# Optimization experiments

Measured on AMD Instinct MI355X. Metric: run time of the kernel, lower is better.

The kernel has to match this reference:

```python
import jax, jax.numpy as jnp
import numpy as np

N, H, W, PD, HID, NH = 2, 64, 64, 16, 128, 4
EPS = 1e-5


def _bn(x, g, b):
    # training-mode BatchNorm over (N, H, W) with biased variance, channels last
    m = jnp.mean(x, axis=(0, 1, 2), keepdims=True)
    v = jnp.var(x, axis=(0, 1, 2), keepdims=True)
    return (x - m) * jax.lax.rsqrt(v + EPS) * g + b


def _mha(x, in_w, in_b, out_w, out_b, nh):
    # torch nn.MultiheadAttention (batch_first) with packed qkv in_proj
    B, S, E = x.shape
    hd = E // nh
    q, k, v = jnp.split(x @ in_w.T + in_b, 3, axis=-1)
    def heads(t):
        return t.reshape(B, S, nh, hd).transpose(0, 2, 1, 3)  # B,nh,S,hd
    q, k, v = heads(q), heads(k), heads(v)
    a = jax.nn.softmax(jnp.einsum('bnqd,bnkd->bnqk', q, k) / np.float32(np.sqrt(hd)), axis=-1)
    o = jnp.einsum('bnqk,bnkd->bnqd', a, v).transpose(0, 2, 1, 3).reshape(B, S, E)
    return o @ out_w.T + out_b


def setup_inputs():
    key = jax.random.key(0)
    ks = jax.random.split(key, 32)
    def r(i, shape, s=0.1):
        return jax.random.normal(ks[i], shape, dtype=jnp.float32) * s
    mask = (jnp.arange(W) % 2) == 0  # alternating columns kept, M = W//2
    return {
        'kspace': jax.random.normal(ks[0], (N, 2, H, W), dtype=jnp.float32),
        'mask': mask,
        'pre_conv_w': r(1, (PD, 2), 0.5), 'pre_conv_b': r(2, (PD,)),
        'pre_pe_H': r(3, (H, PD)), 'pre_pe_W': r(4, (W, PD)),
        'res_conv1_w': r(5, (PD, PD), 0.2), 'res_conv1_b': r(6, (PD,)),
        'res_bn1_g': 1.0 + r(7, (PD,)), 'res_bn1_b': r(8, (PD,)),
        'res_conv2_w': r(9, (PD, PD), 0.2), 'res_conv2_b': r(10, (PD,)),
        'res_bn2_g': 1.0 + r(11, (PD,)), 'res_bn2_b': r(12, (PD,)),
        'proj_w': r(13, (HID, PD), 0.2), 'proj_b': r(14, (HID,)),
        'enc_in_w': r(15, (3 * HID, HID), 0.08), 'enc_in_b': r(16, (3 * HID,)),
        'enc_out_w': r(17, (HID, HID), 0.08), 'enc_out_b': r(18, (HID,)),
        'dec_pe_H': r(19, (H, HID)), 'dec_pe_W': r(20, (W, HID)),
        'dec_in_w': r(21, (3 * HID, HID), 0.08), 'dec_in_b': r(22, (3 * HID,)),
        'dec_out_w': r(23, (HID, HID), 0.08), 'dec_out_b': r(24, (HID,)),
        'masked_token': r(25, (HID,), 1.0),
        'post_w': r(26, (2, HID), 0.1), 'post_b': r(27, (2,)),
    }


def reference(kspace, mask, pre_conv_w, pre_conv_b, pre_pe_H, pre_pe_W,
              res_conv1_w, res_conv1_b, res_bn1_g, res_bn1_b,
              res_conv2_w, res_conv2_b, res_bn2_g, res_bn2_b,
              proj_w, proj_b, enc_in_w, enc_in_b, enc_out_w, enc_out_b,
              dec_pe_H, dec_pe_W, dec_in_w, dec_in_b, dec_out_w, dec_out_b,
              masked_token, post_w, post_b):
    cols = np.nonzero(np.asarray(mask))[0]  # static sampled columns
    M = cols.shape[0]
    # gather valid columns; channels last: [N, H, M, 2]
    x = kspace.transpose(0, 2, 3, 1)[:, :, cols, :]
    h = x @ pre_conv_w.T + pre_conv_b  # 1x1 conv -> [N, H, M, PD]
    h = h + (pre_pe_H[:, None, :] + pre_pe_W[cols][None, :, :])
    # PixelwiseConstantChannelResNet (1 layer)
    r1 = jax.nn.relu(_bn(h @ res_conv1_w.T + res_conv1_b, res_bn1_g, res_bn1_b))
    r2 = jax.nn.relu(_bn(r1 @ res_conv2_w.T + res_conv2_b, res_bn2_g, res_bn2_b))
    h = jax.nn.relu(h + r2)
    h = h @ proj_w.T + proj_b  # [N, H, M, HID]
    enc = _mha(h.reshape(N, H * M, HID), enc_in_w, enc_in_b, enc_out_w, enc_out_b, NH)
    # scatter: fill unmasked positions with masked_token, masked with encoder output
    dec = jnp.broadcast_to(masked_token, (N, H, W, HID))
    dec = dec.at[:, :, cols, :].set(enc.reshape(N, H, M, HID))
    dec = dec + (dec_pe_H[:, None, :] + dec_pe_W[None, :, :])
    dec = _mha(dec.reshape(N, H * W, HID), dec_in_w, dec_in_b, dec_out_w, dec_out_b, NH)
    out = dec.reshape(N, H, W, HID) @ post_w.T + post_b  # [N, H, W, 2]
    return out.transpose(0, 3, 1, 2)  # [N, 2, H, W]
```

## Files before the change

kernel.cpp:

```cpp
#include <hip/hip_runtime.h>
#include <math.h>

#define N_ 2
#define H_ 64
#define W_ 64
#define M_ 32
#define PD_ 16
#define HID_ 128
#define NH_ 4
#define HD_ 32
#define S_ENC 2048
#define S_DEC 4096
#define EPS_ 1e-5f
#define SCALE_ 0.17677669529663687f
#define SCALE2_ (0.17677669529663687f * 1.4426950408889634f)

#define OFF_H     0
#define OFF_T1    65536
#define OFF_T2    131072
#define OFF_STAT  196608
#define OFF_WP    196672
#define OFF_BP    202816
#define OFF_QBF   203264
#define OFF_KBF   727552
#define OFF_VTBF  1251840
#define OFF_ATTBF 1776128
#define OFF_XBF2  2300416
#define OFF_WBF   2824704

#define WOFF_ENC_OUT 0
#define WOFF_DEC_IN  16384
#define WOFF_DEC_OUT 65536

#define IB_MF   2048
#define IB_WC   320
#define IB_WP   24
#define IB_BP   2
#define IB_TOT  (IB_MF + IB_WC + IB_WP + IB_BP + 1)

typedef short bf16x8 __attribute__((ext_vector_type(8)));
typedef short bf16x4 __attribute__((ext_vector_type(4)));
typedef float f32x4 __attribute__((ext_vector_type(4)));

__device__ __forceinline__ short f2bf(float f) {
  union { float f; unsigned u; } v; v.f = f;
  unsigned r = v.u + 0x7FFFu + ((v.u >> 16) & 1u);
  return (short)(r >> 16);
}

__global__ void k_init(const float* __restrict__ eow, const float* __restrict__ dw,
                       const float* __restrict__ dow, const float* __restrict__ mt,
                       const float* __restrict__ peH, const float* __restrict__ peW,
                       const float* __restrict__ ew, const float* __restrict__ pw,
                       const float* __restrict__ pb, const float* __restrict__ eib,
                       short* __restrict__ wbf, short* __restrict__ xdec,
                       float* __restrict__ wp, float* __restrict__ bp,
                       float* __restrict__ stat) {
  int blk = blockIdx.x, tid = threadIdx.x;
  if (blk < IB_MF) {
    int idx = blk * 256 + tid;
    int j = idx & 127;
    int widx = (idx >> 7) & 31;
    int hh = (idx >> 12) & 63;
    int b = idx >> 18;
    int w = 2 * widx + 1;
    xdec[((size_t)(b * 4096 + hh * 64 + w)) * 128 + j] =
        f2bf(mt[j] + peH[hh * 128 + j] + peW[w * 128 + j]);
  } else if (blk < IB_MF + IB_WC) {
    int idx = (blk - IB_MF) * 256 + tid;
    float v;
    if (idx < 16384) v = eow[idx];
    else if (idx < 65536) v = dw[idx - 16384];
    else v = dow[idx - 65536];
    wbf[idx] = f2bf(v);
  } else if (blk < IB_MF + IB_WC + IB_WP) {
    int e = (blk - IB_MF - IB_WC) * 256 + tid;
    int row = e >> 4, k = e & 15;
    float a = 0.f;
    for (int j = 0; j < 128; j++) a = fmaf(ew[row * 128 + j], pw[j * 16 + k], a);
    wp[e] = a;
  } else if (blk < IB_MF + IB_WC + IB_WP + IB_BP) {
    int row = (blk - IB_MF - IB_WC - IB_WP) * 256 + tid;
    if (row < 384) {
      float a = eib[row];
      for (int j = 0; j < 128; j++) a = fmaf(ew[row * 128 + j], pb[j], a);
      bp[row] = a;
    }
  } else {
    if (tid < 64) stat[tid] = 0.f;
  }
}

__global__ void k_prelin_stats(const float* __restrict__ ks, const float* __restrict__ pcw,
                               const float* __restrict__ pcb, const float* __restrict__ peH,
                               const float* __restrict__ peW, const float* __restrict__ w1,
                               const float* __restrict__ b1, float* __restrict__ h,
                               float* __restrict__ t1, float* __restrict__ stat) {
  int tid = threadIdx.x;
  int pos = blockIdx.x * 256 + tid;
  int m = pos & 31, hh = (pos >> 5) & 63, b = pos >> 11;
  int w = 2 * m;
  float x0 = ks[((b * 2 + 0) * H_ + hh) * W_ + w];
  float x1 = ks[((b * 2 + 1) * H_ + hh) * W_ + w];
  float hv[16], tv[16];
#pragma unroll
  for (int c = 0; c < 16; c++)
    hv[c] = x0 * pcw[c * 2] + x1 * pcw[c * 2 + 1] + pcb[c]
            + peH[hh * PD_ + c] + peW[w * PD_ + c];
#pragma unroll
  for (int c = 0; c < 16; c += 4)
    *(float4*)&h[pos * 16 + c] = make_float4(hv[c], hv[c + 1], hv[c + 2], hv[c + 3]);
#pragma unroll
  for (int c = 0; c < 16; c++) {
    float a = b1[c];
#pragma unroll
    for (int k = 0; k < 16; k++) a = fmaf(hv[k], w1[c * 16 + k], a);
    tv[c] = a;
    t1[pos * 16 + c] = a;
  }
  __shared__ float tl[256][17];
#pragma unroll
  for (int c = 0; c < 16; c++) tl[tid][c] = tv[c];
  __syncthreads();
  int c = tid & 15, g = tid >> 4;
  float s = 0.f, s2 = 0.f;
#pragma unroll
  for (int r = 0; r < 16; r++) {
    float v = tl[g * 16 + r][c];
    s += v; s2 += v * v;
  }
  __shared__ float ps[16][16], ps2[16][16];
  ps[g][c] = s; ps2[g][c] = s2;
  __syncthreads();
  if (tid < 16) {
    float S = 0.f, S2 = 0.f;
#pragma unroll
    for (int g2 = 0; g2 < 16; g2++) { S += ps[g2][tid]; S2 += ps2[g2][tid]; }
    atomicAdd(&stat[tid], S);
    atomicAdd(&stat[16 + tid], S2);
  }
}

__global__ void k_bnlin_stats(const float* __restrict__ t1, const float* __restrict__ stat,
                              const float* __restrict__ g1, const float* __restrict__ bb1,
                              const float* __restrict__ w2, const float* __restrict__ b2,
                              float* __restrict__ t2, float* __restrict__ statw) {
  int tid = threadIdx.x;
  int pos = blockIdx.x * 256 + tid;
  const float inv = 1.f / 4096.f;
  float r[16];
#pragma unroll
  for (int k = 0; k < 16; k++) {
    float mu = stat[k] * inv;
    float var = stat[16 + k] * inv - mu * mu;
    float v = (t1[pos * 16 + k] - mu) * rsqrtf(var + EPS_) * g1[k] + bb1[k];
    r[k] = fmaxf(v, 0.f);
  }
  float tv[16];
#pragma unroll
  for (int c = 0; c < 16; c++) {
    float a = b2[c];
#pragma unroll
    for (int k = 0; k < 16; k++) a = fmaf(r[k], w2[c * 16 + k], a);
    tv[c] = a;
    t2[pos * 16 + c] = a;
  }
  __shared__ float tl[256][17];
#pragma unroll
  for (int c = 0; c < 16; c++) tl[tid][c] = tv[c];
  __syncthreads();
  int c = tid & 15, g = tid >> 4;
  float s = 0.f, s2 = 0.f;
#pragma unroll
  for (int rr = 0; rr < 16; rr++) {
    float v = tl[g * 16 + rr][c];
    s += v; s2 += v * v;
  }
  __shared__ float ps[16][16], ps2[16][16];
  ps[g][c] = s; ps2[g][c] = s2;
  __syncthreads();
  if (tid < 16) {
    float S = 0.f, S2 = 0.f;
#pragma unroll
    for (int g2 = 0; g2 < 16; g2++) { S += ps[g2][tid]; S2 += ps2[g2][tid]; }
    atomicAdd(&statw[32 + tid], S);
    atomicAdd(&statw[48 + tid], S2);
  }
}

__global__ __launch_bounds__(256)
void k_fqkv_enc(const float* __restrict__ h, const float* __restrict__ t2,
                const float* __restrict__ stat, const float* __restrict__ g2,
                const float* __restrict__ bb2, const float* __restrict__ wp,
                const float* __restrict__ bp, short* __restrict__ qbf,
                short* __restrict__ kbf, short* __restrict__ vtbf) {
  int tid = threadIdx.x;
  int p0 = blockIdx.x * 32;
  __shared__ float hf[32][20];
  const float inv = 1.f / 4096.f;
#pragma unroll
  for (int i = 0; i < 2; i++) {
    int idx = tid * 2 + i;
    int lp = idx >> 4, c = idx & 15;
    int pos = p0 + lp;
    float mu = stat[32 + c] * inv;
    float var = stat[48 + c] * inv - mu * mu;
    float v = (t2[pos * 16 + c] - mu) * rsqrtf(var + EPS_) * g2[c] + bb2[c];
    v = fmaxf(v, 0.f);
    hf[lp][c] = fmaxf(h[pos * 16 + c] + v, 0.f);
  }
  __syncthreads();
  int bb = p0 >> 11;
  int sbase = p0 & 2047;
  {
    int col = tid;
    float wc[16];
#pragma unroll
    for (int k = 0; k < 16; k += 4) *(float4*)&wc[k] = *(const float4*)&wp[col * 16 + k];
    float bpv = bp[col];
    int isQ = (col < 128);
    int c2 = isQ ? col : (col - 128);
    int hd = c2 >> 5, d = c2 & 31;
    short* dst = isQ ? qbf : kbf;
    float sc = isQ ? SCALE2_ : 1.f;
    size_t rowb = ((size_t)(bb * 4 + hd) * S_ENC + sbase) * 32 + d;
    for (int lp = 0; lp < 32; lp++) {
      float a = bpv;
#pragma unroll
      for (int k = 0; k < 16; k++) a = fmaf(hf[lp][k], wc[k], a);
      dst[rowb + (size_t)lp * 32] = f2bf(a * sc);
    }
  }
  if (tid < 128) {
    int col = 256 + tid;
    float wc[16];
#pragma unroll
    for (int k = 0; k < 16; k += 4) *(float4*)&wc[k] = *(const float4*)&wp[col * 16 + k];
    float bpv = bp[col];
    int c2 = tid;
    int hd = c2 >> 5, d = c2 & 31;
    size_t rowb = ((size_t)(bb * 4 + hd) * 32 + d) * S_ENC + sbase;
    for (int lp4 = 0; lp4 < 32; lp4 += 4) {
      bf16x4 pk;
#pragma unroll
      for (int r = 0; r < 4; r++) {
        float a = bpv;
#pragma unroll
        for (int k = 0; k < 16; k++) a = fmaf(hf[lp4 + r][k], wc[k], a);
        pk[r] = f2bf(a);
      }
      *(bf16x4*)&vtbf[rowb + lp4] = pk;
    }
  }
}

#define MGEMM_STAGE_AND_FRAGS                                                   \
  __shared__ short As[64 * 128];                                                \
  __shared__ short Wl[64 * 128];                                                \
  int tid = threadIdx.x;                                                        \
  _Pragma("unroll")                                                             \
  for (int i = 0; i < 4; i++) {                                                 \
    int idx = i * 256 + tid;                                                    \
    int row = idx >> 4, c = idx & 15, slot = c ^ (row & 7);                     \
    *(bf16x8*)&As[row * 128 + slot * 8] =                                       \
        *(const bf16x8*)&abf[(size_t)(rb + row) * 128 + c * 8];                 \
    *(bf16x8*)&Wl[row * 128 + slot * 8] =                                       \
        *(const bf16x8*)&wbf[(size_t)(ob + row) * 128 + c * 8];                 \
  }                                                                             \
  __syncthreads();                                                              \
  int lane = tid & 63, wv = tid >> 6;                                           \
  int l15 = lane & 15, quad = lane >> 4;                                        \
  int m0 = wv * 16;                                                             \
  f32x4 acc[4];                                                                 \
  acc[0] = acc[1] = acc[2] = acc[3] = (f32x4){0.f, 0.f, 0.f, 0.f};              \
  _Pragma("unroll")                                                             \
  for (int kk = 0; kk < 4; kk++) {                                              \
    int sl = ((kk * 4 + quad) ^ (l15 & 7)) * 8;                                 \
    bf16x8 af = *(const bf16x8*)&As[(m0 + l15) * 128 + sl];                     \
    _Pragma("unroll")                                                           \
    for (int nt = 0; nt < 4; nt++) {                                            \
      bf16x8 wf = *(const bf16x8*)&Wl[(nt * 16 + l15) * 128 + sl];              \
      acc[nt] = __builtin_amdgcn_mfma_f32_16x16x32_bf16(af, wf, acc[nt], 0, 0, 0); \
    }                                                                           \
  }

__global__ __launch_bounds__(256)
void k_mgemm_qkv_dec(const short* __restrict__ abf, const short* __restrict__ wbf,
                     const float* __restrict__ bias, short* __restrict__ qbf,
                     short* __restrict__ kbf, short* __restrict__ vtbf) {
  const int S = 4096;
  int rb = blockIdx.x * 64, ob = blockIdx.y * 64;
  MGEMM_STAGE_AND_FRAGS
#pragma unroll
  for (int nt = 0; nt < 4; nt++) {
    int col = ob + nt * 16 + l15;
    float bv = bias[col];
    if (ob < 128) {
      int hd = col >> 5, d = col & 31;
#pragma unroll
      for (int r = 0; r < 4; r++) {
        int grow = rb + m0 + quad * 4 + r;
        int bb = grow >> 12, s = grow & (S - 1);
        qbf[((size_t)(bb * 4 + hd) * S + s) * 32 + d] =
            f2bf((acc[nt][r] + bv) * SCALE2_);
      }
    } else if (ob < 256) {
      int c2 = col - 128, hd = c2 >> 5, d = c2 & 31;
#pragma unroll
      for (int r = 0; r < 4; r++) {
        int grow = rb + m0 + quad * 4 + r;
        int bb = grow >> 12, s = grow & (S - 1);
        kbf[((size_t)(bb * 4 + hd) * S + s) * 32 + d] = f2bf(acc[nt][r] + bv);
      }
    } else {
      int c2 = col - 256, hd = c2 >> 5, d = c2 & 31;
      int grow0 = rb + m0 + quad * 4;
      int bb = grow0 >> 12, s0 = grow0 & (S - 1);
      bf16x4 pk;
#pragma unroll
      for (int r = 0; r < 4; r++) pk[r] = f2bf(acc[nt][r] + bv);
      *(bf16x4*)&vtbf[((size_t)(bb * 4 + hd) * 32 + d) * S + s0] = pk;
    }
  }
}

__global__ __launch_bounds__(256)
void k_mgemm_out_enc(const short* __restrict__ abf, const short* __restrict__ wbf,
                     const float* __restrict__ bias, const float* __restrict__ peH,
                     const float* __restrict__ peW, short* __restrict__ xdec) {
  int rb = blockIdx.x * 64, ob = blockIdx.y * 64;
  MGEMM_STAGE_AND_FRAGS
#pragma unroll
  for (int nt = 0; nt < 4; nt++) {
    int col = ob + nt * 16 + l15;
    float bv = bias[col];
#pragma unroll
    for (int r = 0; r < 4; r++) {
      int grow = rb + m0 + quad * 4 + r;
      int bb = grow >> 11, rem = grow & 2047;
      int hhh = rem >> 5, m = rem & 31, w = 2 * m;
      xdec[((size_t)(bb * 4096 + hhh * 64 + w)) * 128 + col] =
          f2bf(acc[nt][r] + bv + peH[hhh * 128 + col] + peW[w * 128 + col]);
    }
  }
}

__global__ __launch_bounds__(256)
void k_mgemm_out_post(const short* __restrict__ abf, const short* __restrict__ wbf,
                      const float* __restrict__ bias, const float* __restrict__ pw,
                      const float* __restrict__ pb, float* __restrict__ outp) {
  int rb = blockIdx.x * 64;
  __shared__ short As[64 * 128];
  __shared__ short Wl[128 * 128];
  int tid = threadIdx.x;
#pragma unroll
  for (int i = 0; i < 4; i++) {
    int idx = i * 256 + tid;
    int row = idx >> 4, c = idx & 15, slot = c ^ (row & 7);
    *(bf16x8*)&As[row * 128 + slot * 8] =
        *(const bf16x8*)&abf[(size_t)(rb + row) * 128 + c * 8];
  }
#pragma unroll
  for (int i = 0; i < 8; i++) {
    int idx = i * 256 + tid;
    int row = idx >> 4, c = idx & 15, slot = c ^ (row & 7);
    *(bf16x8*)&Wl[row * 128 + slot * 8] =
        *(const bf16x8*)&wbf[(size_t)row * 128 + c * 8];
  }
  __syncthreads();
  int lane = tid & 63, wv = tid >> 6;
  int l15 = lane & 15, quad = lane >> 4;
  int m0 = wv * 16;
  f32x4 acc[8];
#pragma unroll
  for (int nt = 0; nt < 8; nt++) acc[nt] = (f32x4){0.f, 0.f, 0.f, 0.f};
#pragma unroll
  for (int kk = 0; kk < 4; kk++) {
    int sl = ((kk * 4 + quad) ^ (l15 & 7)) * 8;
    bf16x8 af = *(const bf16x8*)&As[(m0 + l15) * 128 + sl];
#pragma unroll
    for (int nt = 0; nt < 8; nt++) {
      bf16x8 wf = *(const bf16x8*)&Wl[(nt * 16 + l15) * 128 + sl];
      acc[nt] = __builtin_amdgcn_mfma_f32_16x16x32_bf16(af, wf, acc[nt], 0, 0, 0);
    }
  }
  float bv[8], pw0[8], pw1[8];
#pragma unroll
  for (int nt = 0; nt < 8; nt++) {
    int col = nt * 16 + l15;
    bv[nt] = bias[col];
    pw0[nt] = pw[col];
    pw1[nt] = pw[128 + col];
  }
  float pb0 = pb[0], pb1 = pb[1];
#pragma unroll
  for (int r = 0; r < 4; r++) {
    float pc0 = 0.f, pc1 = 0.f;
#pragma unroll
    for (int nt = 0; nt < 8; nt++) {
      float yv = acc[nt][r] + bv[nt];
      pc0 = fmaf(yv, pw0[nt], pc0);
      pc1 = fmaf(yv, pw1[nt], pc1);
    }
    pc0 += __shfl_xor(pc0, 1); pc0 += __shfl_xor(pc0, 2);
    pc0 += __shfl_xor(pc0, 4); pc0 += __shfl_xor(pc0, 8);
    pc1 += __shfl_xor(pc1, 1); pc1 += __shfl_xor(pc1, 2);
    pc1 += __shfl_xor(pc1, 4); pc1 += __shfl_xor(pc1, 8);
    if (l15 == 0) {
      int grow = rb + m0 + quad * 4 + r;
      int bb = grow >> 12, hw = grow & 4095;
      outp[(size_t)(bb * 2 + 0) * 4096 + hw] = pc0 + pb0;
      outp[(size_t)(bb * 2 + 1) * 4096 + hw] = pc1 + pb1;
    }
  }
}

template <int S>
__global__ __launch_bounds__(1024)
__attribute__((amdgpu_waves_per_eu(8)))
void k_attn11(const short* __restrict__ qbf, const short* __restrict__ kbf,
              const short* __restrict__ vtbf, short* __restrict__ outb) {
  __shared__ __align__(16) char smem[65536];
  short* kb4 = (short*)smem;
  short* vt4 = (short*)(smem + 16384);
  short* pb4 = (short*)(smem + 32768);
  float* abuf = (float*)smem;
  float* lb   = (float*)(smem + 24576);

  int qt = blockIdx.x, hh = blockIdx.y, b = blockIdx.z;
  int tid = threadIdx.x;
  int lane = tid & 63;
  int wv = tid >> 6;
  int qtr = wv >> 2;
  int wv4 = wv & 3;
  int l15 = lane & 15, quad = lane >> 4;
  int t256 = tid & 255;

  int bh = b * NH_ + hh;
  const short* kg = kbf + (size_t)bh * S * 32;
  const short* vg = vtbf + (size_t)bh * 32 * S;
  short* kbh = kb4 + qtr * 2048;
  short* vth = vt4 + qtr * 2048;

  bf16x8 qf = *(const bf16x8*)&qbf[((size_t)bh * S + qt * 64 + wv4 * 16 + l15) * 32
                                   + quad * 8];

  f32x4 acc[2];
  acc[0] = (f32x4){0.f, 0.f, 0.f, 0.f};
  acc[1] = (f32x4){0.f, 0.f, 0.f, 0.f};
  float lpart = 0.f;

  int srowK = t256 >> 2, schK = t256 & 3;
  int slotK = schK ^ (srowK & 3);
  int srowV = t256 >> 3, sslV = t256 & 7;
  int sgV = sslV ^ (srowV & 7);

  short* prow = pb4 + (size_t)(qtr * 64 + wv4 * 16 + l15) * 64;
  int kq0 = qtr * (S / 4);
  int kxor = l15 & 3;
  int pxor = l15 & 7;

  for (int it = 0; it < S / 256; ++it) {
    int ktg = kq0 + it * 64;
    __syncthreads();
    *(bf16x8*)&kbh[srowK * 32 + slotK * 8] =
        *(const bf16x8*)&kg[(size_t)(ktg + srowK) * 32 + schK * 8];
    *(bf16x8*)&vth[srowV * 64 + sslV * 8] =
        *(const bf16x8*)&vg[(size_t)srowV * S + ktg + sgV * 8];
    __syncthreads();

    f32x4 s[4];
#pragma unroll
    for (int t = 0; t < 4; t++) {
      bf16x8 kf = *(const bf16x8*)&kbh[(t * 16 + l15) * 32 + ((quad ^ kxor) * 8)];
      s[t] = __builtin_amdgcn_mfma_f32_16x16x32_bf16(
          kf, qf, (f32x4){0.f, 0.f, 0.f, 0.f}, 0, 0, 0);
    }

#pragma unroll
    for (int t = 0; t < 4; t++) {
      float p0 = __builtin_exp2f(s[t][0]);
      float p1 = __builtin_exp2f(s[t][1]);
      float p2 = __builtin_exp2f(s[t][2]);
      float p3 = __builtin_exp2f(s[t][3]);
      lpart += (p0 + p1) + (p2 + p3);
      unsigned a0 = __float_as_uint(p0) + 0x8000u;
      unsigned a1 = __float_as_uint(p1) + 0x8000u;
      unsigned a2 = __float_as_uint(p2) + 0x8000u;
      unsigned a3 = __float_as_uint(p3) + 0x8000u;
      uint2 pk;
      pk.x = __builtin_amdgcn_perm(a1, a0, 0x07060302u);
      pk.y = __builtin_amdgcn_perm(a3, a2, 0x07060302u);
      int cc = t * 2 + (quad >> 1);
      *(uint2*)&prow[(cc ^ pxor) * 8 + (quad & 1) * 4] = pk;
    }

#pragma unroll
    for (int kh = 0; kh < 2; kh++) {
      int cc2 = kh * 4 + quad;
      bf16x8 pf = *(const bf16x8*)&prow[(cc2 ^ pxor) * 8];
#pragma unroll
      for (int nt = 0; nt < 2; nt++) {
        bf16x8 vf = *(const bf16x8*)&vth[(nt * 16 + l15) * 64 + ((cc2 ^ pxor) * 8)];
        acc[nt] = __builtin_amdgcn_mfma_f32_16x16x32_bf16(vf, pf, acc[nt], 0, 0, 0);
      }
    }
  }

  lpart += __shfl_xor(lpart, 16);
  lpart += __shfl_xor(lpart, 32);

  __syncthreads();
  if (qtr > 0) {
#pragma unroll
    for (int nt = 0; nt < 2; nt++)
#pragma unroll
      for (int r = 0; r < 4; r++)
        abuf[(qtr - 1) * 2048 + wv4 * 512 + (nt * 16 + quad * 4 + r) * 16 + l15] =
            acc[nt][r];
    if (quad == 0) lb[(qtr - 1) * 64 + wv4 * 16 + l15] = lpart;
  }
  __syncthreads();
  if (qtr == 0) {
    int li = wv4 * 16 + l15;
    float ltot = lpart + lb[li] + lb[64 + li] + lb[128 + li];
    float inv = 1.f / ltot;
    int base = wv4 * 512;
    short* op = outb + ((size_t)(b * S + qt * 64 + wv4 * 16 + l15)) * 128 + hh * 32;
#pragma unroll
    for (int nt = 0; nt < 2; nt++) {
      bf16x4 pk;
#pragma unroll
      for (int r = 0; r < 4; r++) {
        int d = nt * 16 + quad * 4 + r;
        float v = acc[nt][r] + abuf[base + d * 16 + l15]
                + abuf[2048 + base + d * 16 + l15]
                + abuf[4096 + base + d * 16 + l15];
        pk[r] = f2bf(v * inv);
      }
      *(bf16x4*)&op[nt * 16 + quad * 4] = pk;
    }
  }
}

extern "C" void kernel_launch(void* const* d_in, const int* in_sizes, int n_in,
                              void* d_out, int out_size, void* d_ws, size_t ws_size,
                              hipStream_t stream) {
  const float* ks        = (const float*)d_in[0];
  const float* pre_conv_w = (const float*)d_in[2];
  const float* pre_conv_b = (const float*)d_in[3];
  const float* pre_pe_H   = (const float*)d_in[4];
  const float* pre_pe_W   = (const float*)d_in[5];
  const float* w1  = (const float*)d_in[6];
  const float* b1  = (const float*)d_in[7];
  const float* g1  = (const float*)d_in[8];
  const float* bb1 = (const float*)d_in[9];
  const float* w2  = (const float*)d_in[10];
  const float* b2  = (const float*)d_in[11];
  const float* g2  = (const float*)d_in[12];
  const float* bb2 = (const float*)d_in[13];
  const float* proj_w = (const float*)d_in[14];
  const float* proj_b = (const float*)d_in[15];
  const float* enc_in_w  = (const float*)d_in[16];
  const float* enc_in_b  = (const float*)d_in[17];
  const float* enc_out_w = (const float*)d_in[18];
  const float* enc_out_b = (const float*)d_in[19];
  const float* dec_pe_H  = (const float*)d_in[20];
  const float* dec_pe_W  = (const float*)d_in[21];
  const float* dec_in_w  = (const float*)d_in[22];
  const float* dec_in_b  = (const float*)d_in[23];
  const float* dec_out_w = (const float*)d_in[24];
  const float* dec_out_b = (const float*)d_in[25];
  const float* masked_token = (const float*)d_in[26];
  const float* post_w = (const float*)d_in[27];
  const float* post_b = (const float*)d_in[28];
  float* out = (float*)d_out;

  float* ws    = (float*)d_ws;
  float* h     = ws + OFF_H;
  float* t1    = ws + OFF_T1;
  float* t2    = ws + OFF_T2;
  float* stat  = ws + OFF_STAT;
  float* wp    = ws + OFF_WP;
  float* bp    = ws + OFF_BP;
  short* qbf   = (short*)(ws + OFF_QBF);
  short* kbfb  = (short*)(ws + OFF_KBF);
  short* vtbfb = (short*)(ws + OFF_VTBF);
  short* attbf = (short*)(ws + OFF_ATTBF);
  short* xbf2  = (short*)(ws + OFF_XBF2);
  short* wbf   = (short*)(ws + OFF_WBF);

  k_init<<<IB_TOT, 256, 0, stream>>>(enc_out_w, dec_in_w, dec_out_w, masked_token,
                                     dec_pe_H, dec_pe_W, enc_in_w, proj_w, proj_b,
                                     enc_in_b, wbf, xbf2, wp, bp, stat);
  k_prelin_stats<<<16, 256, 0, stream>>>(ks, pre_conv_w, pre_conv_b, pre_pe_H,
                                         pre_pe_W, w1, b1, h, t1, stat);
  k_bnlin_stats<<<16, 256, 0, stream>>>(t1, stat, g1, bb1, w2, b2, t2, stat);
  k_fqkv_enc<<<128, 256, 0, stream>>>(h, t2, stat, g2, bb2, wp, bp,
                                      qbf, kbfb, vtbfb);
  k_attn11<S_ENC><<<dim3(S_ENC / 64, NH_, N_), 1024, 0, stream>>>(qbf, kbfb, vtbfb, attbf);
  k_mgemm_out_enc<<<dim3(S_ENC * N_ / 64, 2), 256, 0, stream>>>(
      attbf, wbf + WOFF_ENC_OUT, enc_out_b, dec_pe_H, dec_pe_W, xbf2);
  k_mgemm_qkv_dec<<<dim3(S_DEC * N_ / 64, 6), 256, 0, stream>>>(
      xbf2, wbf + WOFF_DEC_IN, dec_in_b, qbf, kbfb, vtbfb);
  k_attn11<S_DEC><<<dim3(S_DEC / 64, NH_, N_), 1024, 0, stream>>>(qbf, kbfb, vtbfb, attbf);
  k_mgemm_out_post<<<S_DEC * N_ / 64, 256, 0, stream>>>(
      attbf, wbf + WOFF_DEC_OUT, dec_out_b, post_w, post_b, out);
}
```

Before: 222.4 us.

## Prefetch next K/V tile into registers, fix LDS swizzle, use packed bf16 convert

```diff
diff --git a/kernel.cpp b/kernel.cpp
--- a/kernel.cpp
+++ b/kernel.cpp
@@ -451,23 +451,39 @@
   float lpart = 0.f;
 
   int srowK = t256 >> 2, schK = t256 & 3;
-  int slotK = schK ^ (srowK & 3);
+  int slotK = schK ^ ((srowK >> 1) & 3);
   int srowV = t256 >> 3, sslV = t256 & 7;
   int sgV = sslV ^ (srowV & 7);
 
   short* prow = pb4 + (size_t)(qtr * 64 + wv4 * 16 + l15) * 64;
   int kq0 = qtr * (S / 4);
-  int kxor = l15 & 3;
+  int kxor = (l15 >> 1) & 3;
   int pxor = l15 & 7;
 
-  for (int it = 0; it < S / 256; ++it) {
-    int ktg = kq0 + it * 64;
-    __syncthreads();
-    *(bf16x8*)&kbh[srowK * 32 + slotK * 8] =
-        *(const bf16x8*)&kg[(size_t)(ktg + srowK) * 32 + schK * 8];
-    *(bf16x8*)&vth[srowV * 64 + sslV * 8] =
-        *(const bf16x8*)&vg[(size_t)srowV * S + ktg + sgV * 8];
-    __syncthreads();
+  const short* kgp = kg + (size_t)(kq0 + srowK) * 32 + schK * 8;
+  const short* vgp = vg + (size_t)srowV * S + kq0 + sgV * 8;
+  short* kdst = kbh + srowK * 32 + slotK * 8;
+  short* vdst = vth + srowV * 64 + sslV * 8;
+
+  bf16x8 krg = *(const bf16x8*)kgp;
+  bf16x8 vrg = *(const bf16x8*)vgp;
+
+  constexpr int NIT = S / 256;
+  for (int it = 0; it < NIT; ++it) {
+    asm volatile("s_waitcnt lgkmcnt(0)" ::: "memory");
+    __builtin_amdgcn_s_barrier();
+    asm volatile("" ::: "memory");
+    *(bf16x8*)kdst = krg;
+    *(bf16x8*)vdst = vrg;
+    if (it + 1 < NIT) {
+      kgp += 64 * 32;
+      vgp += 64;
+      krg = *(const bf16x8*)kgp;
+      vrg = *(const bf16x8*)vgp;
+    }
+    asm volatile("s_waitcnt lgkmcnt(0)" ::: "memory");
+    __builtin_amdgcn_s_barrier();
+    asm volatile("" ::: "memory");
 
     f32x4 s[4];
 #pragma unroll
@@ -484,13 +500,12 @@
       float p2 = __builtin_exp2f(s[t][2]);
       float p3 = __builtin_exp2f(s[t][3]);
       lpart += (p0 + p1) + (p2 + p3);
-      unsigned a0 = __float_as_uint(p0) + 0x8000u;
-      unsigned a1 = __float_as_uint(p1) + 0x8000u;
-      unsigned a2 = __float_as_uint(p2) + 0x8000u;
-      unsigned a3 = __float_as_uint(p3) + 0x8000u;
+      unsigned w0, w1;
+      asm("v_cvt_pk_bf16_f32 %0, %1, %2" : "=v"(w0) : "v"(p0), "v"(p1));
+      asm("v_cvt_pk_bf16_f32 %0, %1, %2" : "=v"(w1) : "v"(p2), "v"(p3));
       uint2 pk;
-      pk.x = __builtin_amdgcn_perm(a1, a0, 0x07060302u);
-      pk.y = __builtin_amdgcn_perm(a3, a2, 0x07060302u);
+      pk.x = w0;
+      pk.y = w1;
       int cc = t * 2 + (quad >> 1);
       *(uint2*)&prow[(cc ^ pxor) * 8 + (quad & 1) * 4] = pk;
     }
```

Result: faster. 210.4 us (-5.4%).
